# Kernel tuning notes

Measured on AMD Instinct MI355X. Metric: run time of the kernel, lower is better.

The kernel has to match this reference:

```python
import jax, jax.numpy as jnp
import numpy as np

NUM_HEADS = 12
EMB = 768
HEAD = 64
SEQ = 2048
BATCH = 2


def setup_inputs() -> dict:
    key = jax.random.key(0)
    ks = jax.random.split(key, 6)
    scale = 0.02
    x = jax.random.normal(ks[0], (BATCH, SEQ, EMB), dtype=jnp.float32)
    # per-head Q/K/V projections (bias-free, Karpathy-style HeadAttention), batched over heads
    Wq = jax.random.normal(ks[1], (NUM_HEADS, EMB, HEAD), dtype=jnp.float32) * scale
    Wk = jax.random.normal(ks[2], (NUM_HEADS, EMB, HEAD), dtype=jnp.float32) * scale
    Wv = jax.random.normal(ks[3], (NUM_HEADS, EMB, HEAD), dtype=jnp.float32) * scale
    # output projection: Linear(head_size*num_heads, emb_size)
    Wo = jax.random.normal(ks[4], (NUM_HEADS * HEAD, EMB), dtype=jnp.float32) * scale
    bo = jax.random.normal(ks[5], (EMB,), dtype=jnp.float32) * scale
    return {"x": x, "Wq": Wq, "Wk": Wk, "Wv": Wv, "Wo": Wo, "bo": bo}


def reference(x, Wq, Wk, Wv, Wo, bo):
    B, S, E = x.shape
    # batched per-head projections: [B,S,E] x [H,E,D] -> [B,H,S,D]
    q = jnp.einsum("bse,hed->bhsd", x, Wq)
    k = jnp.einsum("bse,hed->bhsd", x, Wk)
    v = jnp.einsum("bse,hed->bhsd", x, Wv)
    scale = 1.0 / jnp.sqrt(jnp.asarray(HEAD, dtype=x.dtype))
    scores = jnp.einsum("bhsd,bhtd->bhst", q, k) * scale  # [B,H,S,S]
    causal = jnp.tril(jnp.ones((S, S), dtype=bool))
    scores = jnp.where(causal, scores, jnp.asarray(-jnp.inf, dtype=scores.dtype))
    attn = jax.nn.softmax(scores, axis=-1)
    out = jnp.einsum("bhst,bhtd->bhsd", attn, v)  # [B,H,S,D]
    # concat heads along last dim: [B,S,H*D]
    out = out.transpose(0, 2, 1, 3).reshape(B, S, NUM_HEADS * HEAD)
    # output projection (dropout is identity in eval mode)
    return out @ Wo + bo
```

## Files before the change

### kernel.cpp

```cpp
#include <hip/hip_runtime.h>
#include <hip/hip_bf16.h>
#include <string.h>

#define NHEAD 12
#define EMB 768
#define HDD 64
#define SEQ 2048

typedef __attribute__((ext_vector_type(4))) float f32x4;
typedef __attribute__((ext_vector_type(8))) short short8;
typedef __attribute__((ext_vector_type(4))) short short4v;
typedef __attribute__((ext_vector_type(2))) unsigned uint2v;
typedef unsigned int u32;

#define GLL16(g, l)                                                            \
    __builtin_amdgcn_global_load_lds(                                          \
        (const __attribute__((address_space(1))) u32*)(g),                     \
        (__attribute__((address_space(3))) u32*)(l), 16, 0, 0)

static __device__ __forceinline__ short bf16s(float f) {
    unsigned u = __builtin_bit_cast(unsigned, f);
    u = (u + 0x7fffu + ((u >> 16) & 1u)) >> 16;
    return (short)u;
}
static __device__ __forceinline__ float bf2f(short s) {
    unsigned u = ((unsigned)(unsigned short)s) << 16;
    return __builtin_bit_cast(float, u);
}
static __device__ __forceinline__ float ex2(float x) {
    float r;
    asm("v_exp_f32 %0, %1" : "=v"(r) : "v"(x));
    return r;
}
static __device__ __forceinline__ unsigned pk2(float a, float b) {
    float2 f2;
    f2.x = a;
    f2.y = b;
    __hip_bfloat162 h = __float22bfloat162_rn(f2);
    unsigned r;
    memcpy(&r, &h, 4);
    return r;
}

__global__ void k_cvt_all(const float* __restrict__ x, const float* __restrict__ Wq,
                          const float* __restrict__ Wk, const float* __restrict__ Wv,
                          const float* __restrict__ Wo, short* __restrict__ xb,
                          short* __restrict__ WqT, short* __restrict__ WkT,
                          short* __restrict__ WvT, short* __restrict__ WoT) {
    const int bid = blockIdx.x, t = threadIdx.x;
    if (bid < 1536) {
        const int i = (bid * 256 + t) * 8;
        const f32x4* s = (const f32x4*)(x + i);
        f32x4 a = s[0], b = s[1];
        short8 o;
        o[0] = bf16s(a[0]); o[1] = bf16s(a[1]); o[2] = bf16s(a[2]); o[3] = bf16s(a[3]);
        o[4] = bf16s(b[0]); o[5] = bf16s(b[1]); o[6] = bf16s(b[2]); o[7] = bf16s(b[3]);
        *(short8*)(xb + i) = o;
    } else if (bid < 1968) {
        const int idx = bid - 1536;
        const int h = idx % 12, e0 = ((idx / 12) % 12) * 64, z = idx / 144;
        const float* W = z == 0 ? Wq : (z == 1 ? Wk : Wv);
        short* Wt = z == 0 ? WqT : (z == 1 ? WkT : WvT);
        __shared__ float tile[64][65];
        const int r = t >> 2, c0 = (t & 3) * 16;
        const float* src = W + (h * EMB + e0 + r) * HDD + c0;
#pragma unroll
        for (int i = 0; i < 16; ++i) tile[r][c0 + i] = src[i];
        __syncthreads();
        short* dst = Wt + (h * HDD + r) * EMB + e0 + c0;
#pragma unroll
        for (int i = 0; i < 16; ++i) dst[i] = bf16s(tile[c0 + i][r]);
    } else {
        const int idx = bid - 1968;
        const int k0 = (idx % 12) * 64, n0 = (idx / 12) * 64;
        __shared__ float tile[64][65];
        const int r = t >> 2, c0 = (t & 3) * 16;
        const float* src = Wo + (k0 + r) * EMB + n0 + c0;
#pragma unroll
        for (int i = 0; i < 16; ++i) tile[r][c0 + i] = src[i];
        __syncthreads();
        short* dst = WoT + (n0 + r) * EMB + k0 + c0;
#pragma unroll
        for (int i = 0; i < 16; ++i) dst[i] = bf16s(tile[c0 + i][r]);
    }
}

template <int MODE>
__global__ __launch_bounds__(256) void k_gemm(
        const short* __restrict__ xb, const short* __restrict__ Wt0,
        const short* __restrict__ Wt1, const short* __restrict__ Wt2,
        short* __restrict__ Qo, short* __restrict__ Ko, short* __restrict__ Vo,
        const float* __restrict__ bias, float* __restrict__ Fout) {
    __shared__ alignas(16) short As[128 * 32];
    __shared__ alignas(16) short Bs[128 * 32];
    const int t = threadIdx.x, lane = t & 63, wave = t >> 6;
    const int z = (MODE == 0) ? blockIdx.z : 0;
    const short* Ap;
    const short* Bp;
    int m0, n0;
    if (MODE == 1) {
        Ap = xb; Bp = Wt0; m0 = blockIdx.y * 128; n0 = blockIdx.x * 128;
    } else if (z == 0) {
        Ap = xb; Bp = Wt0; m0 = blockIdx.y * 128; n0 = blockIdx.x * 128;
    } else if (z == 1) {
        Ap = xb; Bp = Wt1; m0 = blockIdx.y * 128; n0 = blockIdx.x * 128;
    } else {
        Ap = Wt2; Bp = xb; m0 = blockIdx.x * 128; n0 = blockIdx.y * 128;
    }

    const int srow = lane >> 2;
    const int scolSw = ((lane & 3) ^ ((srow >> 1) & 3)) * 8;
    const short* gA = Ap + (long)(m0 + wave * 32 + srow) * EMB + scolSw;
    const short* gB = Bp + (long)(n0 + wave * 32 + srow) * EMB + scolSw;
    short* lA = As + (wave * 32) * 32;
    short* lB = Bs + (wave * 32) * 32;

    const int wm = (wave >> 1) * 64, wn = (wave & 1) * 64;
    const int fr = lane & 15, hi = lane >> 4;
    const int rdoff = (hi ^ ((fr >> 1) & 3)) * 8;

    f32x4 acc[4][4];
#pragma unroll
    for (int i = 0; i < 4; ++i)
#pragma unroll
        for (int j = 0; j < 4; ++j)
#pragma unroll
            for (int e = 0; e < 4; ++e) acc[i][j][e] = 0.f;

    for (int kk = 0; kk < EMB; kk += 32) {
        __syncthreads();
        GLL16(gA + kk, lA);
        GLL16(gA + kk + 16 * EMB, lA + 16 * 32);
        GLL16(gB + kk, lB);
        GLL16(gB + kk + 16 * EMB, lB + 16 * 32);
        __syncthreads();
        short8 af[4], bfq[4];
#pragma unroll
        for (int i = 0; i < 4; ++i)
            af[i] = *(const short8*)(As + (wm + i * 16 + fr) * 32 + rdoff);
#pragma unroll
        for (int j = 0; j < 4; ++j)
            bfq[j] = *(const short8*)(Bs + (wn + j * 16 + fr) * 32 + rdoff);
#pragma unroll
        for (int i = 0; i < 4; ++i)
#pragma unroll
            for (int j = 0; j < 4; ++j)
                acc[i][j] = __builtin_amdgcn_mfma_f32_16x16x32_bf16(af[i], bfq[j], acc[i][j], 0, 0, 0);
    }

    const int r0 = hi * 4;
#pragma unroll
    for (int i = 0; i < 4; ++i) {
#pragma unroll
        for (int j = 0; j < 4; ++j) {
            const int nbase = n0 + wn + j * 16 + fr;
            float bj = 0.f;
            if (MODE == 1) bj = bias[nbase];
#pragma unroll
            for (int r = 0; r < 4; ++r) {
                const int m = m0 + wm + i * 16 + r0 + r;
                float v = acc[i][j][r];
                if (MODE == 0) {
                    if (z == 2) {
                        const int hh = m >> 6, dd = m & 63;
                        const int bb = nbase >> 11, ss = nbase & 2047;
                        Vo[(long)((bb * NHEAD + hh) * HDD + dd) * SEQ + ss] = bf16s(v);
                    } else {
                        const int bb = m >> 11, ss = m & 2047;
                        const int hh = nbase >> 6, dd = nbase & 63;
                        short* Dst = (z == 0) ? Qo : Ko;
                        if (z == 0) v *= 0.18033688f;
                        Dst[(long)((bb * NHEAD + hh) * SEQ + ss) * HDD + dd] = bf16s(v);
                    }
                } else {
                    Fout[(long)m * EMB + nbase] = v + bj;
                }
            }
        }
    }
}

__global__ __launch_bounds__(256) void k_attn(
        const short* __restrict__ Q, const short* __restrict__ K,
        const short* __restrict__ VT, short* __restrict__ O,
        short* __restrict__ Ub, float* __restrict__ Mb, float* __restrict__ Lb) {
    __shared__ alignas(16) short Kbuf[2][64 * 72];
    __shared__ alignas(16) short Vbuf[2][64 * 72];
    __shared__ alignas(16) short Ps[4][16 * 72];
    const int bh = blockIdx.x;
    const int h = bh % NHEAD, b = bh / NHEAD;
    const int yy = blockIdx.y;
    int qs, kb, ke, chunk, split;
    if (yy < 16)      { qs = 16 + yy; kb = 0;  ke = 16;     chunk = 0; split = 1; }
    else if (yy < 32) { qs = yy;      kb = 16; ke = qs + 1; chunk = 1; split = 1; }
    else              { qs = 47 - yy; kb = 0;  ke = qs + 1; chunk = 0; split = 0; }
    const int q0 = qs * 64;
    const int t = threadIdx.x, lane = t & 63, wave = t >> 6;
    const long base = (long)(b * NHEAD + h) * SEQ * HDD;
    const short* Qg = Q + base;
    const short* Kg = K + base;
    const short* Vg = VT + base;
    const int fr = lane & 15, hi = lane >> 4, fk = hi * 8, r0 = hi * 4;
    const int wq = q0 + wave * 16;

    short8 qf[2];
#pragma unroll
    for (int c = 0; c < 2; ++c)
        qf[c] = *(const short8*)(Qg + (long)(wq + fr) * HDD + c * 32 + fk);

    f32x4 oacc[4];
#pragma unroll
    for (int i = 0; i < 4; ++i)
#pragma unroll
        for (int e = 0; e < 4; ++e) oacc[i][e] = 0.f;
    float mrun = -3e38f, lrun = 0.f;

    const int srow = t >> 2, sc = (t & 3) * 16;
    const short* KgS = Kg + (long)srow * HDD + sc;
    const short* VgS = Vg + (long)srow * SEQ + sc;
    short* Pw = &Ps[wave][0];

    short8 kv0 = *(const short8*)(KgS + (long)(kb * 64) * HDD);
    short8 kv1 = *(const short8*)(KgS + (long)(kb * 64) * HDD + 8);
    short8 vv0 = *(const short8*)(VgS + kb * 64);
    short8 vv1 = *(const short8*)(VgS + kb * 64 + 8);
    *(short8*)(&Kbuf[0][srow * 72 + sc]) = kv0;
    *(short8*)(&Kbuf[0][srow * 72 + sc + 8]) = kv1;
    *(short8*)(&Vbuf[0][srow * 72 + sc]) = vv0;
    *(short8*)(&Vbuf[0][srow * 72 + sc + 8]) = vv1;
    if (ke - kb > 1) {
        kv0 = *(const short8*)(KgS + (long)(kb * 64 + 64) * HDD);
        kv1 = *(const short8*)(KgS + (long)(kb * 64 + 64) * HDD + 8);
        vv0 = *(const short8*)(VgS + kb * 64 + 64);
        vv1 = *(const short8*)(VgS + kb * 64 + 64 + 8);
    }
    __syncthreads();

    for (int kt = kb; kt < ke; ++kt) {
        const int k0 = kt * 64;
        const int cur = (kt - kb) & 1;
        if (kt + 1 < ke) {
            *(short8*)(&Kbuf[cur ^ 1][srow * 72 + sc]) = kv0;
            *(short8*)(&Kbuf[cur ^ 1][srow * 72 + sc + 8]) = kv1;
            *(short8*)(&Vbuf[cur ^ 1][srow * 72 + sc]) = vv0;
            *(short8*)(&Vbuf[cur ^ 1][srow * 72 + sc + 8]) = vv1;
            if (kt + 2 < ke) {
                kv0 = *(const short8*)(KgS + (long)(k0 + 128) * HDD);
                kv1 = *(const short8*)(KgS + (long)(k0 + 128) * HDD + 8);
                vv0 = *(const short8*)(VgS + (k0 + 128));
                vv1 = *(const short8*)(VgS + (k0 + 128) + 8);
            }
        }
        if (k0 <= wq + 15) {
            const short* Ks = &Kbuf[cur][0];
            const short* Vs = &Vbuf[cur][0];

            f32x4 st[4];
#pragma unroll
            for (int nt = 0; nt < 4; ++nt) {
                const short8 kf0 = *(const short8*)(Ks + (nt * 16 + fr) * 72 + fk);
                const short8 kf1 = *(const short8*)(Ks + (nt * 16 + fr) * 72 + 32 + fk);
#pragma unroll
                for (int e = 0; e < 4; ++e) st[nt][e] = 0.f;
                st[nt] = __builtin_amdgcn_mfma_f32_16x16x32_bf16(kf0, qf[0], st[nt], 0, 0, 0);
                st[nt] = __builtin_amdgcn_mfma_f32_16x16x32_bf16(kf1, qf[1], st[nt], 0, 0, 0);
            }

            float p[4][4];
            float pmax = -3e38f;
            if (k0 + 63 > wq) {
                const int myq = wq + fr;
#pragma unroll
                for (int nt = 0; nt < 4; ++nt)
#pragma unroll
                    for (int r = 0; r < 4; ++r) {
                        float s = st[nt][r];
                        if (k0 + nt * 16 + r0 + r > myq) s = -3e38f;
                        p[nt][r] = s;
                        pmax = fmaxf(pmax, s);
                    }
            } else {
#pragma unroll
                for (int nt = 0; nt < 4; ++nt)
#pragma unroll
                    for (int r = 0; r < 4; ++r) {
                        p[nt][r] = st[nt][r];
                        pmax = fmaxf(pmax, st[nt][r]);
                    }
            }
            pmax = fmaxf(pmax, __shfl_xor(pmax, 16, 64));
            pmax = fmaxf(pmax, __shfl_xor(pmax, 32, 64));
            const float mnew = fmaxf(mrun, pmax);
            const float corr = ex2(mrun - mnew);
            mrun = mnew;
            float rsum = 0.f;
#pragma unroll
            for (int nt = 0; nt < 4; ++nt)
#pragma unroll
                for (int r = 0; r < 4; ++r) {
                    const float e = ex2(p[nt][r] - mnew);
                    p[nt][r] = e;
                    rsum += e;
                }
            rsum += __shfl_xor(rsum, 16, 64);
            rsum += __shfl_xor(rsum, 32, 64);
            lrun = lrun * corr + rsum;
#pragma unroll
            for (int dt = 0; dt < 4; ++dt)
#pragma unroll
                for (int e = 0; e < 4; ++e) oacc[dt][e] *= corr;

#pragma unroll
            for (int nt = 0; nt < 4; ++nt) {
                uint2v w;
                w[0] = pk2(p[nt][0], p[nt][1]);
                w[1] = pk2(p[nt][2], p[nt][3]);
                *(uint2v*)(Pw + fr * 72 + nt * 16 + r0) = w;
            }

#pragma unroll
            for (int kc = 0; kc < 2; ++kc) {
                const short8 pf = *(const short8*)(Pw + fr * 72 + kc * 32 + fk);
#pragma unroll
                for (int dt = 0; dt < 4; ++dt) {
                    const short8 vf = *(const short8*)(Vs + (dt * 16 + fr) * 72 + kc * 32 + fk);
                    oacc[dt] = __builtin_amdgcn_mfma_f32_16x16x32_bf16(vf, pf, oacc[dt], 0, 0, 0);
                }
            }
        }
        __syncthreads();
    }

    if (split) {
        const int pidx = (bh * 16 + (qs - 16)) * 2 + chunk;
        short* Up = Ub + pidx * 4096;
#pragma unroll
        for (int dt = 0; dt < 4; ++dt)
#pragma unroll
            for (int r = 0; r < 4; ++r)
                Up[(dt * 16 + r0 + r) * 64 + wave * 16 + fr] = bf16s(oacc[dt][r]);
        if (lane < 16) {
            Mb[pidx * 64 + wave * 16 + lane] = mrun;
            Lb[pidx * 64 + wave * 16 + lane] = lrun;
        }
        return;
    }

    short* Os = &Ps[0][0];
    const float iv = 1.0f / lrun;
#pragma unroll
    for (int dt = 0; dt < 4; ++dt) {
        uint2v w;
        w[0] = pk2(oacc[dt][0] * iv, oacc[dt][1] * iv);
        w[1] = pk2(oacc[dt][2] * iv, oacc[dt][3] * iv);
        *(uint2v*)(Os + (wave * 16 + fr) * 72 + dt * 16 + r0) = w;
    }
    __syncthreads();
    {
        const int row = t >> 2, c0 = (t & 3) * 16;
        const short8 o0 = *(const short8*)(Os + row * 72 + c0);
        const short8 o1 = *(const short8*)(Os + row * 72 + c0 + 8);
        short* Og = O + (long)(b * SEQ + q0 + row) * EMB + h * HDD + c0;
        *(short8*)Og = o0;
        *(short8*)(Og + 8) = o1;
    }
}

__global__ __launch_bounds__(256) void k_merge(
        const short* __restrict__ Ub, const float* __restrict__ Mb,
        const float* __restrict__ Lb, short* __restrict__ O) {
    __shared__ float aS[64], bS[64], iL[64];
    __shared__ short tile[64 * 72];
    const int bid = blockIdx.x;
    const int bh = bid >> 4, sidx = bid & 15;
    const int h = bh % NHEAD, b = bh / NHEAD;
    const int q0 = (16 + sidx) * 64;
    const int p0 = (bh * 16 + sidx) * 2, p1 = p0 + 1;
    const int t = threadIdx.x;
    if (t < 64) {
        const float m1 = Mb[p0 * 64 + t], m2 = Mb[p1 * 64 + t];
        const float l1 = Lb[p0 * 64 + t], l2 = Lb[p1 * 64 + t];
        const float m = fmaxf(m1, m2);
        const float a = ex2(m1 - m), bb = ex2(m2 - m);
        aS[t] = a;
        bS[t] = bb;
        iL[t] = 1.0f / (l1 * a + l2 * bb);
    }
    __syncthreads();
    {
        const int d = t >> 2, qg = (t & 3) * 16;
        const short8 u1a = *(const short8*)(Ub + p0 * 4096 + d * 64 + qg);
        const short8 u1b = *(const short8*)(Ub + p0 * 4096 + d * 64 + qg + 8);
        const short8 u2a = *(const short8*)(Ub + p1 * 4096 + d * 64 + qg);
        const short8 u2b = *(const short8*)(Ub + p1 * 4096 + d * 64 + qg + 8);
#pragma unroll
        for (int i = 0; i < 8; ++i) {
            const int q = qg + i;
            tile[q * 72 + d] = bf16s((bf2f(u1a[i]) * aS[q] + bf2f(u2a[i]) * bS[q]) * iL[q]);
        }
#pragma unroll
        for (int i = 0; i < 8; ++i) {
            const int q = qg + 8 + i;
            tile[q * 72 + d] = bf16s((bf2f(u1b[i]) * aS[q] + bf2f(u2b[i]) * bS[q]) * iL[q]);
        }
    }
    __syncthreads();
    {
        const int q = t >> 2, dg = (t & 3) * 16;
        const short8 o0 = *(const short8*)(tile + q * 72 + dg);
        const short8 o1 = *(const short8*)(tile + q * 72 + dg + 8);
        short* Og = O + (long)(b * SEQ + q0 + q) * EMB + h * HDD + dg;
        *(short8*)Og = o0;
        *(short8*)(Og + 8) = o1;
    }
}

extern "C" void kernel_launch(void* const* d_in, const int* in_sizes, int n_in,
                              void* d_out, int out_size, void* d_ws, size_t ws_size,
                              hipStream_t stream) {
    const float* x  = (const float*)d_in[0];
    const float* Wq = (const float*)d_in[1];
    const float* Wk = (const float*)d_in[2];
    const float* Wv = (const float*)d_in[3];
    const float* Wo = (const float*)d_in[4];
    const float* bo = (const float*)d_in[5];
    float* out = (float*)d_out;

    char* ws = (char*)d_ws;
    short* xb  = (short*)(ws + 0);
    short* WqT = (short*)(ws + 6291456);
    short* WkT = (short*)(ws + 7471104);
    short* WvT = (short*)(ws + 8650752);
    short* WoT = (short*)(ws + 9830400);
    short* Qb  = (short*)(ws + 11010048);
    short* Kb  = (short*)(ws + 17301504);
    short* VTb = (short*)(ws + 23592960);
    short* Ob  = (short*)(ws + 29884416);
    short* Ub  = (short*)(ws + 0);
    float* Mb  = (float*)(ws + 6291456);
    float* Lb  = (float*)(ws + 6488064);

    k_cvt_all<<<dim3(2112), dim3(256), 0, stream>>>(
        x, Wq, Wk, Wv, Wo, xb, WqT, WkT, WvT, WoT);
    k_gemm<0><<<dim3(6, 32, 3), dim3(256), 0, stream>>>(
        xb, WqT, WkT, WvT, Qb, Kb, VTb, (const float*)nullptr, (float*)nullptr);
    k_attn<<<dim3(24, 48), dim3(256), 0, stream>>>(Qb, Kb, VTb, Ob, Ub, Mb, Lb);
    k_merge<<<dim3(384), dim3(256), 0, stream>>>(Ub, Mb, Lb, Ob);
    k_gemm<1><<<dim3(6, 32, 1), dim3(256), 0, stream>>>(
        Ob, WoT, (const short*)nullptr, (const short*)nullptr,
        (short*)nullptr, (short*)nullptr, (short*)nullptr, bo, out);
}
```

Before: 96.10 us.

## Fuse Q/K/V projections per head into one GEMM kernel with LDS-transposed V store

```diff
diff --git a/kernel.cpp b/kernel.cpp
--- a/kernel.cpp
+++ b/kernel.cpp
@@ -85,33 +85,119 @@
     }
 }
 
-template <int MODE>
-__global__ __launch_bounds__(256) void k_gemm(
-        const short* __restrict__ xb, const short* __restrict__ Wt0,
-        const short* __restrict__ Wt1, const short* __restrict__ Wt2,
-        short* __restrict__ Qo, short* __restrict__ Ko, short* __restrict__ Vo,
+__global__ __launch_bounds__(256) void k_gemmqkv(
+        const short* __restrict__ xb, const short* __restrict__ WqT,
+        const short* __restrict__ WkT, const short* __restrict__ WvT,
+        short* __restrict__ Qo, short* __restrict__ Ko, short* __restrict__ Vo) {
+    __shared__ alignas(16) short As[128 * 32];
+    __shared__ alignas(16) short Bs[3][64 * 32];
+    __shared__ alignas(16) short Tb[64 * 136];
+    const int t = threadIdx.x, lane = t & 63, wave = t >> 6;
+    const int hh = blockIdx.x;
+    const int n0 = hh * HDD;
+    const int m0 = blockIdx.y * 128;
+
+    const int srow = t >> 2;
+    const int scolSw = ((t & 3) ^ ((srow >> 1) & 3)) * 8;
+    const short* gA0 = xb + (long)(m0 + srow) * EMB + scolSw;
+    const short* gA1 = xb + (long)(m0 + 64 + srow) * EMB + scolSw;
+    const short* gBq = WqT + (long)(n0 + srow) * EMB + scolSw;
+    const short* gBk = WkT + (long)(n0 + srow) * EMB + scolSw;
+    const short* gBv = WvT + (long)(n0 + srow) * EMB + scolSw;
+    short* lA0 = As + (wave * 16) * 32;
+    short* lA1 = As + (64 + wave * 16) * 32;
+    short* lBq = &Bs[0][(wave * 16) * 32];
+    short* lBk = &Bs[1][(wave * 16) * 32];
+    short* lBv = &Bs[2][(wave * 16) * 32];
+
+    const int fr = lane & 15, hi = lane >> 4;
+    const int rdoff = (hi ^ ((fr >> 1) & 3)) * 8;
+
+    f32x4 acc[3][2][4];
+#pragma unroll
+    for (int z = 0; z < 3; ++z)
+#pragma unroll
+        for (int i = 0; i < 2; ++i)
+#pragma unroll
+            for (int j = 0; j < 4; ++j)
+#pragma unroll
+                for (int e = 0; e < 4; ++e) acc[z][i][j][e] = 0.f;
+
+    for (int kk = 0; kk < EMB; kk += 32) {
+        __syncthreads();
+        GLL16(gA0 + kk, lA0);
+        GLL16(gA1 + kk, lA1);
+        GLL16(gBq + kk, lBq);
+        GLL16(gBk + kk, lBk);
+        GLL16(gBv + kk, lBv);
+        __syncthreads();
+        short8 af[2], bq[4], bk[4], bv[4];
+#pragma unroll
+        for (int i = 0; i < 2; ++i)
+            af[i] = *(const short8*)(As + (wave * 32 + i * 16 + fr) * 32 + rdoff);
+#pragma unroll
+        for (int j = 0; j < 4; ++j) {
+            bq[j] = *(const short8*)(&Bs[0][(j * 16 + fr) * 32 + rdoff]);
+            bk[j] = *(const short8*)(&Bs[1][(j * 16 + fr) * 32 + rdoff]);
+            bv[j] = *(const short8*)(&Bs[2][(j * 16 + fr) * 32 + rdoff]);
+        }
+#pragma unroll
+        for (int i = 0; i < 2; ++i)
+#pragma unroll
+            for (int j = 0; j < 4; ++j) {
+                acc[0][i][j] = __builtin_amdgcn_mfma_f32_16x16x32_bf16(af[i], bq[j], acc[0][i][j], 0, 0, 0);
+                acc[1][i][j] = __builtin_amdgcn_mfma_f32_16x16x32_bf16(af[i], bk[j], acc[1][i][j], 0, 0, 0);
+                acc[2][i][j] = __builtin_amdgcn_mfma_f32_16x16x32_bf16(af[i], bv[j], acc[2][i][j], 0, 0, 0);
+            }
+    }
+
+    const int r0 = hi * 4;
+    const int bb = m0 >> 11, sbase = m0 & 2047;
+    const long qkbase = ((long)(bb * NHEAD + hh) * SEQ + sbase) * HDD;
+#pragma unroll
+    for (int i = 0; i < 2; ++i) {
+#pragma unroll
+        for (int j = 0; j < 4; ++j) {
+            const int dd = j * 16 + fr;
+#pragma unroll
+            for (int r = 0; r < 4; ++r) {
+                const int sl = wave * 32 + i * 16 + r0 + r;
+                Qo[qkbase + (long)sl * HDD + dd] = bf16s(acc[0][i][j][r] * 0.18033688f);
+                Ko[qkbase + (long)sl * HDD + dd] = bf16s(acc[1][i][j][r]);
+            }
+        }
+    }
+#pragma unroll
+    for (int i = 0; i < 2; ++i)
+#pragma unroll
+        for (int j = 0; j < 4; ++j)
+#pragma unroll
+            for (int r = 0; r < 4; ++r)
+                Tb[(j * 16 + fr) * 136 + wave * 32 + i * 16 + r0 + r] = bf16s(acc[2][i][j][r]);
+    __syncthreads();
+    {
+        const int dd = t >> 2, sc = (t & 3) * 32;
+        short* dst = Vo + ((long)(bb * NHEAD + hh) * HDD + dd) * SEQ + sbase + sc;
+        const short* src = Tb + dd * 136 + sc;
+        *(short8*)(dst) = *(const short8*)(src);
+        *(short8*)(dst + 8) = *(const short8*)(src + 8);
+        *(short8*)(dst + 16) = *(const short8*)(src + 16);
+        *(short8*)(dst + 24) = *(const short8*)(src + 24);
+    }
+}
+
+__global__ __launch_bounds__(256) void k_gemmo(
+        const short* __restrict__ Ob, const short* __restrict__ WoT,
         const float* __restrict__ bias, float* __restrict__ Fout) {
     __shared__ alignas(16) short As[128 * 32];
     __shared__ alignas(16) short Bs[128 * 32];
     const int t = threadIdx.x, lane = t & 63, wave = t >> 6;
-    const int z = (MODE == 0) ? blockIdx.z : 0;
-    const short* Ap;
-    const short* Bp;
-    int m0, n0;
-    if (MODE == 1) {
-        Ap = xb; Bp = Wt0; m0 = blockIdx.y * 128; n0 = blockIdx.x * 128;
-    } else if (z == 0) {
-        Ap = xb; Bp = Wt0; m0 = blockIdx.y * 128; n0 = blockIdx.x * 128;
-    } else if (z == 1) {
-        Ap = xb; Bp = Wt1; m0 = blockIdx.y * 128; n0 = blockIdx.x * 128;
-    } else {
-        Ap = Wt2; Bp = xb; m0 = blockIdx.x * 128; n0 = blockIdx.y * 128;
-    }
+    const int m0 = blockIdx.y * 128, n0 = blockIdx.x * 128;
 
     const int srow = lane >> 2;
     const int scolSw = ((lane & 3) ^ ((srow >> 1) & 3)) * 8;
-    const short* gA = Ap + (long)(m0 + wave * 32 + srow) * EMB + scolSw;
-    const short* gB = Bp + (long)(n0 + wave * 32 + srow) * EMB + scolSw;
+    const short* gA = Ob + (long)(m0 + wave * 32 + srow) * EMB + scolSw;
+    const short* gB = WoT + (long)(n0 + wave * 32 + srow) * EMB + scolSw;
     short* lA = As + (wave * 32) * 32;
     short* lB = Bs + (wave * 32) * 32;
 
@@ -154,27 +240,11 @@
 #pragma unroll
         for (int j = 0; j < 4; ++j) {
             const int nbase = n0 + wn + j * 16 + fr;
-            float bj = 0.f;
-            if (MODE == 1) bj = bias[nbase];
+            const float bj = bias[nbase];
 #pragma unroll
             for (int r = 0; r < 4; ++r) {
                 const int m = m0 + wm + i * 16 + r0 + r;
-                float v = acc[i][j][r];
-                if (MODE == 0) {
-                    if (z == 2) {
-                        const int hh = m >> 6, dd = m & 63;
-                        const int bb = nbase >> 11, ss = nbase & 2047;
-                        Vo[(long)((bb * NHEAD + hh) * HDD + dd) * SEQ + ss] = bf16s(v);
-                    } else {
-                        const int bb = m >> 11, ss = m & 2047;
-                        const int hh = nbase >> 6, dd = nbase & 63;
-                        short* Dst = (z == 0) ? Qo : Ko;
-                        if (z == 0) v *= 0.18033688f;
-                        Dst[(long)((bb * NHEAD + hh) * SEQ + ss) * HDD + dd] = bf16s(v);
-                    }
-                } else {
-                    Fout[(long)m * EMB + nbase] = v + bj;
-                }
+                Fout[(long)m * EMB + nbase] = acc[i][j][r] + bj;
             }
         }
     }
@@ -442,11 +512,9 @@
 
     k_cvt_all<<<dim3(2112), dim3(256), 0, stream>>>(
         x, Wq, Wk, Wv, Wo, xb, WqT, WkT, WvT, WoT);
-    k_gemm<0><<<dim3(6, 32, 3), dim3(256), 0, stream>>>(
-        xb, WqT, WkT, WvT, Qb, Kb, VTb, (const float*)nullptr, (float*)nullptr);
+    k_gemmqkv<<<dim3(12, 32), dim3(256), 0, stream>>>(
+        xb, WqT, WkT, WvT, Qb, Kb, VTb);
     k_attn<<<dim3(24, 48), dim3(256), 0, stream>>>(Qb, Kb, VTb, Ob, Ub, Mb, Lb);
     k_merge<<<dim3(384), dim3(256), 0, stream>>>(Ub, Mb, Lb, Ob);
-    k_gemm<1><<<dim3(6, 32, 1), dim3(256), 0, stream>>>(
-        Ob, WoT, (const short*)nullptr, (const short*)nullptr,
-        (short*)nullptr, (short*)nullptr, (short*)nullptr, bo, out);
-}
+    k_gemmo<<<dim3(6, 32), dim3(256), 0, stream>>>(Ob, WoT, bo, out);
+}
```

After: 100.4 us. +4.5%, slower.
